# Kernel optimization log

Hardware: AMD Instinct MI355X
Metric: run time of the kernel (lower is better)

## Reference

```python
import jax, jax.numpy as jnp
import numpy as np

N_NODES = 100000
D = 128
ATT = 128
P_EDGE_TYPES = 3
N_EDGES = 1600000
BATCH = 65536


def gcn_conv(x, W, b, src, dst, n):
    # PyG GCNConv: add self loops, symmetric D^{-1/2} (A+I) D^{-1/2} x W + b
    h = x @ W                                   # [N, D]
    ones = jnp.ones(src.shape[0], x.dtype)
    deg = jax.ops.segment_sum(ones, dst, num_segments=n) + 1.0  # +1 self loop
    dinv = jax.lax.rsqrt(deg)
    norm = dinv[src] * dinv[dst]                # [E]
    out = jax.ops.segment_sum(h[src] * norm[:, None], dst, num_segments=n)
    out = out + h * (dinv * dinv)[:, None]      # self-loop message, norm = dinv_i^2
    return out + b


def semantic_attention(z, P, W, b, q):
    # z: [P*N, D] -> per-edge-type scalar attention, softmax over P, weighted sum
    att = jnp.tanh(z @ W + b) @ q               # [P*N]
    att = att.reshape(P, -1).mean(axis=1)       # [P]
    att = jax.nn.softmax(att)
    zp = z.reshape(P, -1, z.shape[-1])          # [P, N, D]
    return jnp.einsum('p,pnd->nd', att, zp)     # [N, D]


def gnn_branch(x0, edge_index, W1, b1, W2, b2, n):
    outs = []
    for t in range(edge_index.shape[0]):        # fixed small set of edge types
        src, dst = edge_index[t, 0], edge_index[t, 1]
        h = jax.nn.relu(gcn_conv(x0, W1, b1, src, dst, n))
        h = jax.nn.relu(gcn_conv(h, W2, b2, src, dst, n))
        outs.append(h)
    return jnp.concatenate(outs, axis=0)        # [P*N, D]


def setup_inputs() -> dict:
    key = jax.random.key(0)
    ks = jax.random.split(key, 16)
    x = jax.random.normal(ks[0], (N_NODES, D), jnp.float32)
    edge_index = jax.random.randint(ks[1], (P_EDGE_TYPES, 2, N_EDGES), 0, N_NODES, jnp.int64)
    perm = jax.random.permutation(ks[2], N_NODES).astype(jnp.int64)
    summary_vetor = jax.random.normal(ks[3], (D,), jnp.float32)
    s = 1.0 / np.sqrt(D)
    params = dict(
        W_lin=jax.random.normal(ks[4], (D, D), jnp.float32) * s,
        b_lin=jnp.zeros((D,), jnp.float32),
        W1=jax.random.normal(ks[5], (D, D), jnp.float32) * s,
        b1=jnp.zeros((D,), jnp.float32),
        W2=jax.random.normal(ks[6], (D, D), jnp.float32) * s,
        b2=jnp.zeros((D,), jnp.float32),
        W_sem=jax.random.normal(ks[7], (D, ATT), jnp.float32) * s,
        b_sem=jnp.zeros((ATT,), jnp.float32),
        q_sem=jax.random.normal(ks[8], (ATT,), jnp.float32) * (1.0 / np.sqrt(ATT)),
        W_disc=jax.random.normal(ks[9], (D, D), jnp.float32) * s,
        b_disc=jnp.zeros((), jnp.float32),
    )
    return dict(x=x, edge_index=edge_index, perm=perm,
                summary_vetor=summary_vetor, Batch_size=BATCH, **params)


def reference(x, edge_index, perm, summary_vetor, Batch_size,
              W_lin, b_lin, W1, b1, W2, b2, W_sem, b_sem, q_sem, W_disc, b_disc):
    n = x.shape[0]
    x_pos = jax.nn.relu(x @ W_lin + b_lin)
    x_neg = jax.nn.relu(x[perm] @ W_lin + b_lin)

    z_pos = gnn_branch(x_pos, edge_index, W1, b1, W2, b2, n)
    z_neg = gnn_branch(x_neg, edge_index, W1, b1, W2, b2, n)

    P = edge_index.shape[0]
    att_pos = semantic_attention(z_pos, P, W_sem, b_sem, q_sem)[:Batch_size]
    att_neg = semantic_attention(z_neg, P, W_sem, b_sem, q_sem)[:Batch_size]

    summary_in = att_pos.mean(axis=0)           # AvgReadout
    summary = 0.5 * (summary_vetor + summary_in)

    # Discriminator: bilinear score against broadcast summary
    c = W_disc @ summary                        # [D]
    sc_pos = att_pos @ c + b_disc               # [B]
    sc_neg = att_neg @ c + b_disc               # [B]
    ret = jnp.concatenate([sc_pos, sc_neg], axis=0)  # [2B]
    return ret, summary
```

## Files before the change

### kernel.cpp

```cpp
#include <hip/hip_runtime.h>

#define D_ 128
#define BATCH_ 65536
#define BSH 10
#define TILE_ 16384

typedef _Float16 f16;
typedef _Float16 h2v __attribute__((ext_vector_type(2)));
typedef _Float16 h4v __attribute__((ext_vector_type(4)));
typedef _Float16 f16x8 __attribute__((ext_vector_type(8)));
typedef float f32x4 __attribute__((ext_vector_type(4)));

__global__ void k_zero32(uint32_t* p, long long n) {
    long long i = (long long)blockIdx.x * blockDim.x + threadIdx.x;
    long long st = (long long)gridDim.x * blockDim.x;
    for (; i < n; i += st) p[i] = 0u;
}

__global__ void k_sentinel(float* p, long long n) {
    long long i = (long long)blockIdx.x * blockDim.x + threadIdx.x;
    long long st = (long long)gridDim.x * blockDim.x;
    for (; i < n; i += st) p[i] = -12345.0f;
}

__global__ void k_wt(const float* __restrict__ W, f16* __restrict__ Wt) {
    int t = blockIdx.x * 256 + threadIdx.x;
    int k = t >> 7, c = t & 127;
    Wt[c * 128 + k] = (f16)W[k * 128 + c];
}

__global__ void k_gath(const uint32_t* __restrict__ src, const int* __restrict__ perm,
                       uint32_t* __restrict__ dst, int N) {
    int i = blockIdx.x * 256 + threadIdx.x;
    if (i >= N * 64) return;
    int row = i >> 6, col = i & 63;
    dst[i] = src[((size_t)perm[row] << 6) + col];
}

__global__ void k_hist(const int* __restrict__ ei, int* __restrict__ bcnt,
                       int E, int nbt, int nbuk) {
    __shared__ int hist[512];
    for (int i = threadIdx.x; i < 512; i += 256) hist[i] = 0;
    __syncthreads();
    long long tot = 3LL * E;
    long long i = (long long)blockIdx.x * 256 + threadIdx.x;
    long long st = (long long)gridDim.x * 256;
    for (; i < tot; i += st) {
        int t = (i >= E) + (i >= 2LL * E);
        long long w = i - (long long)t * E;
        int dst = ei[(long long)t * 2 * E + E + w];
        atomicAdd(&hist[t * nbt + (dst >> BSH)], 1);
    }
    __syncthreads();
    for (int i2 = threadIdx.x; i2 < nbuk; i2 += 256)
        if (hist[i2]) atomicAdd(&bcnt[i2], hist[i2]);
}

__global__ void k_bscan(const int* __restrict__ bcnt, int* __restrict__ bbase,
                        int* __restrict__ bcur, int nbuk) {
    __shared__ int s[512];
    int t = threadIdx.x;
    int v = (t < nbuk) ? bcnt[t] : 0;
    s[t] = v;
    __syncthreads();
    for (int off = 1; off < 512; off <<= 1) {
        int a = (t >= off) ? s[t - off] : 0;
        __syncthreads();
        s[t] += a;
        __syncthreads();
    }
    if (t < nbuk) {
        int e = s[t] - v;
        bbase[t] = e;
        bcur[t] = e;
        if (t == nbuk - 1) bbase[nbuk] = s[t];
    }
}

__global__ __launch_bounds__(256) void k_scatter(const int* __restrict__ ei,
                                                 int* __restrict__ bcur,
                                                 uint32_t* __restrict__ pairs,
                                                 int E, int nbt, int nbuk) {
    __shared__ int hist[512];
    __shared__ int base[512];
    long long tot = 3LL * E;
    long long w0 = (long long)blockIdx.x * TILE_;
    long long w1 = w0 + TILE_ < tot ? w0 + TILE_ : tot;
    for (int i = threadIdx.x; i < 512; i += 256) hist[i] = 0;
    __syncthreads();
    for (long long e = w0 + threadIdx.x; e < w1; e += 256) {
        int t = (e >= E) + (e >= 2LL * E);
        long long w = e - (long long)t * E;
        int dst = ei[(long long)t * 2 * E + E + w];
        atomicAdd(&hist[t * nbt + (dst >> BSH)], 1);
    }
    __syncthreads();
    for (int i = threadIdx.x; i < nbuk; i += 256) {
        int c = hist[i];
        base[i] = c ? atomicAdd(&bcur[i], c) : 0;
        hist[i] = 0;
    }
    __syncthreads();
    for (long long e = w0 + threadIdx.x; e < w1; e += 256) {
        int t = (e >= E) + (e >= 2LL * E);
        long long w = e - (long long)t * E;
        int src = ei[(long long)t * 2 * E + w];
        int dst = ei[(long long)t * 2 * E + E + w];
        int b = t * nbt + (dst >> BSH);
        int off = atomicAdd(&hist[b], 1);
        pairs[base[b] + off] = (uint32_t)src | ((uint32_t)(dst & ((1 << BSH) - 1)) << 22);
    }
}

__global__ __launch_bounds__(256) void k_bucket(const uint32_t* __restrict__ pairs,
                                                const int* __restrict__ bbase,
                                                int* __restrict__ rowstart,
                                                float* __restrict__ dinv,
                                                int* __restrict__ csr,
                                                int N, int nbt, int nbuk, int L) {
    __shared__ int cnt[1024];
    __shared__ int pref[1024];
    __shared__ int sums[256];
    int b = blockIdx.x;
    int t = b / nbt, bb = b - t * nbt;
    int dst0 = bb << BSH;
    int ndst = (N - dst0 < 1024) ? (N - dst0) : 1024;
    int e0 = bbase[b], e1 = bbase[b + 1];
    int tid = threadIdx.x;
    for (int i = tid; i < 1024; i += 256) cnt[i] = 0;
    __syncthreads();
    for (int e = e0 + tid; e < e1; e += 256) atomicAdd(&cnt[pairs[e] >> 22], 1);
    __syncthreads();
    int i0 = tid * 4;
    int c0 = cnt[i0], c1 = cnt[i0 + 1], c2 = cnt[i0 + 2], c3 = cnt[i0 + 3];
    int s4 = c0 + c1 + c2 + c3;
    sums[tid] = s4;
    __syncthreads();
    for (int off = 1; off < 256; off <<= 1) {
        int v = (tid >= off) ? sums[tid - off] : 0;
        __syncthreads();
        sums[tid] += v;
        __syncthreads();
    }
    int run = sums[tid] - s4;
    pref[i0] = run; run += c0;
    pref[i0 + 1] = run; run += c1;
    pref[i0 + 2] = run; run += c2;
    pref[i0 + 3] = run;
    __syncthreads();
    for (int d = tid; d < ndst; d += 256) {
        int r = t * N + dst0 + d;
        rowstart[r] = e0 + pref[d];
        dinv[r] = rsqrtf((float)cnt[d] + 1.0f);
    }
    if (b == nbuk - 1 && tid == 0) rowstart[L] = e1;
    __syncthreads();
    for (int e = e0 + tid; e < e1; e += 256) {
        uint32_t u = pairs[e];
        int d = u >> 22;
        int pos = e0 + atomicAdd(&pref[d], 1);
        csr[pos] = (int)(u & ((1u << 22) - 1));
    }
}

__global__ void k_wedge(const int* __restrict__ csr, const float* __restrict__ dinv,
                        f16* __restrict__ w16, int N, int E) {
    long long tot = 3LL * E;
    long long i = (long long)blockIdx.x * 256 + threadIdx.x;
    long long st = (long long)gridDim.x * 256;
    for (; i < tot; i += st) {
        int t = (i >= E) + (i >= 2LL * E);
        w16[i] = (f16)dinv[t * N + csr[i]];
    }
}

__global__ __launch_bounds__(256) void k_mgemm(const void* __restrict__ in, int in_f32,
                                               const f16* __restrict__ Wt,
                                               const float* __restrict__ bias,
                                               f16* __restrict__ outh, int n, int relu) {
    int l = threadIdx.x & 63, wid = threadIdx.x >> 6;
    int row0 = blockIdx.x * 64 + wid * 16;
    int r = l & 15, kg = l >> 4;
    int arow = row0 + r;
    f32x4 acc[8] = {};
#pragma unroll
    for (int kk = 0; kk < 4; kk++) {
        int off = kk * 32 + kg * 8;
        f16x8 a = {};
        if (arow < n) {
            if (in_f32) {
                const float* inf = (const float*)in + (size_t)arow * D_ + off;
                float4 v0 = *(const float4*)inf;
                float4 v1 = *(const float4*)(inf + 4);
                a[0] = (f16)v0.x; a[1] = (f16)v0.y; a[2] = (f16)v0.z; a[3] = (f16)v0.w;
                a[4] = (f16)v1.x; a[5] = (f16)v1.y; a[6] = (f16)v1.z; a[7] = (f16)v1.w;
            } else {
                a = *(const f16x8*)((const f16*)in + (size_t)arow * D_ + off);
            }
        }
#pragma unroll
        for (int ct = 0; ct < 8; ct++) {
            int c = ct * 16 + r;
            f16x8 b = *(const f16x8*)(Wt + (size_t)c * D_ + off);
            acc[ct] = __builtin_amdgcn_mfma_f32_16x16x32_f16(a, b, acc[ct], 0, 0, 0);
        }
    }
#pragma unroll
    for (int ct = 0; ct < 8; ct++) {
        int c = ct * 16 + r;
        float bs = bias ? bias[c] : 0.0f;
#pragma unroll
        for (int j = 0; j < 4; j++) {
            int rr = row0 + kg * 4 + j;
            if (rr >= n) continue;
            float o = acc[ct][j] + bs;
            if (relu) o = fmaxf(o, 0.0f);
            outh[(size_t)rr * D_ + c] = (f16)o;
        }
    }
}

__global__ __launch_bounds__(256) void k_matt(const f16* __restrict__ z,
                                              const f16* __restrict__ Wst,
                                              const float* __restrict__ bsem,
                                              const float* __restrict__ q,
                                              float* __restrict__ att_part, int n, int ttype) {
    int l = threadIdx.x & 63, wid = threadIdx.x >> 6;
    int row0 = blockIdx.x * 64 + wid * 16;
    int r = l & 15, kg = l >> 4;
    int arow = row0 + r;
    f32x4 acc[8] = {};
#pragma unroll
    for (int kk = 0; kk < 4; kk++) {
        int off = kk * 32 + kg * 8;
        f16x8 a = {};
        if (arow < n) a = *(const f16x8*)(z + (size_t)arow * D_ + off);
#pragma unroll
        for (int ct = 0; ct < 8; ct++) {
            int c = ct * 16 + r;
            f16x8 b = *(const f16x8*)(Wst + (size_t)c * D_ + off);
            acc[ct] = __builtin_amdgcn_mfma_f32_16x16x32_f16(a, b, acc[ct], 0, 0, 0);
        }
    }
    float s = 0.0f;
#pragma unroll
    for (int ct = 0; ct < 8; ct++) {
        int c = ct * 16 + r;
        float qc = q[c], bc = bsem[c];
#pragma unroll
        for (int j = 0; j < 4; j++) {
            int rr = row0 + kg * 4 + j;
            if (rr < n) s += qc * tanhf(acc[ct][j] + bc);
        }
    }
#pragma unroll
    for (int m = 1; m < 64; m <<= 1) s += __shfl_xor(s, m, 64);
    __shared__ float ws[4];
    if (l == 0) ws[wid] = s;
    __syncthreads();
    if (threadIdx.x == 0)
        atomicAdd(&att_part[((blockIdx.x & 63) << 2) + ttype], ws[0] + ws[1] + ws[2] + ws[3]);
}

__global__ __launch_bounds__(256) void k_spmm(const f16* __restrict__ gsrc,
                                              const int* __restrict__ csr,
                                              const f16* __restrict__ w16,
                                              const int* __restrict__ rowstart,
                                              const float* __restrict__ dinv,
                                              const float* __restrict__ bias,
                                              f16* __restrict__ outh,
                                              int N, int rows, int src_typed) {
    int tid = (int)threadIdx.x;
    int lp = tid & 15;
    int gw = blockIdx.x * 16 + (tid >> 4);
    if (gw >= rows) return;
    int t = (gw >= N) + (gw >= 2 * N);
    int tbase = t * N;
    int sbase = src_typed ? tbase : 0;
    int self = src_typed ? gw : gw - tbase;
    int s0 = rowstart[gw], s1 = rowstart[gw + 1];
    float di = dinv[gw];
    size_t co = (size_t)(lp << 3);
    const f16* gp = gsrc + co;
    float a[8];
    {
        f16x8 sv = *(const f16x8*)(gp + (size_t)self * D_);
#pragma unroll
        for (int u = 0; u < 8; u++) a[u] = (float)sv[u] * di;
    }
    int j = s0;
    for (; j + 2 <= s1; j += 2) {
        int sA = csr[j], sB = csr[j + 1];
        float wA = (float)w16[j], wB = (float)w16[j + 1];
        f16x8 vA = *(const f16x8*)(gp + (size_t)(sbase + sA) * D_);
        f16x8 vB = *(const f16x8*)(gp + (size_t)(sbase + sB) * D_);
#pragma unroll
        for (int u = 0; u < 8; u++) a[u] = fmaf((float)vA[u], wA, a[u]);
#pragma unroll
        for (int u = 0; u < 8; u++) a[u] = fmaf((float)vB[u], wB, a[u]);
    }
    if (j < s1) {
        int s = csr[j];
        float w = (float)w16[j];
        f16x8 v = *(const f16x8*)(gp + (size_t)(sbase + s) * D_);
#pragma unroll
        for (int u = 0; u < 8; u++) a[u] = fmaf((float)v[u], w, a[u]);
    }
    float4 b0 = *(const float4*)(bias + co);
    float4 b1 = *(const float4*)(bias + co + 4);
    f16x8 o;
    o[0] = (f16)fmaxf(fmaf(a[0], di, b0.x), 0.f);
    o[1] = (f16)fmaxf(fmaf(a[1], di, b0.y), 0.f);
    o[2] = (f16)fmaxf(fmaf(a[2], di, b0.z), 0.f);
    o[3] = (f16)fmaxf(fmaf(a[3], di, b0.w), 0.f);
    o[4] = (f16)fmaxf(fmaf(a[4], di, b1.x), 0.f);
    o[5] = (f16)fmaxf(fmaf(a[5], di, b1.y), 0.f);
    o[6] = (f16)fmaxf(fmaf(a[6], di, b1.z), 0.f);
    o[7] = (f16)fmaxf(fmaf(a[7], di, b1.w), 0.f);
    *(f16x8*)(outh + (size_t)gw * D_ + co) = o;
}

__global__ void k_attw(const float* __restrict__ att_part, float* __restrict__ att_w, float invN) {
    __shared__ float sb[3];
    int t = threadIdx.x;
    if (t < 3) {
        float s = 0.f;
        for (int i = 0; i < 64; i++) s += att_part[(i << 2) + t];
        sb[t] = s * invN;
    }
    __syncthreads();
    if (t == 0) {
        float m = fmaxf(sb[0], fmaxf(sb[1], sb[2]));
        float x0 = expf(sb[0] - m), x1 = expf(sb[1] - m), x2 = expf(sb[2] - m);
        float inv = 1.f / (x0 + x1 + x2);
        att_w[0] = x0 * inv; att_w[1] = x1 * inv; att_w[2] = x2 * inv;
    }
}

__global__ __launch_bounds__(256) void k_colsum(const f16* __restrict__ Z, size_t tstride,
                                                const float* __restrict__ att_w,
                                                float* __restrict__ colsum) {
    int c2 = threadIdx.x & 63;
    int rg = threadIdx.x >> 6;
    int nbase = blockIdx.x << 7;
    float w0 = att_w[0], w1 = att_w[1], w2 = att_w[2];
    float csx = 0.f, csy = 0.f;
    for (int i = rg; i < 128; i += 4) {
        size_t off = (size_t)(nbase + i) * D_ + (c2 << 1);
        h2v z0 = *(const h2v*)(Z + off);
        h2v z1 = *(const h2v*)(Z + tstride + off);
        h2v z2 = *(const h2v*)(Z + 2 * tstride + off);
        csx += w0 * (float)z0.x + w1 * (float)z1.x + w2 * (float)z2.x;
        csy += w0 * (float)z0.y + w1 * (float)z1.y + w2 * (float)z2.y;
    }
    __shared__ float red[4][128];
    red[rg][c2 << 1] = csx;
    red[rg][(c2 << 1) + 1] = csy;
    __syncthreads();
    if (rg == 0) {
        float sx = red[0][c2 << 1] + red[1][c2 << 1] + red[2][c2 << 1] + red[3][c2 << 1];
        float sy = red[0][(c2 << 1) + 1] + red[1][(c2 << 1) + 1] + red[2][(c2 << 1) + 1] + red[3][(c2 << 1) + 1];
        atomicAdd(&colsum[c2 << 1], sx);
        atomicAdd(&colsum[(c2 << 1) + 1], sy);
    }
}

__global__ void k_summary_c(const float* __restrict__ colsum, const float* __restrict__ sv,
                            const float* __restrict__ Wd, float* __restrict__ cvec,
                            float* __restrict__ out_summary) {
    __shared__ float sl[128];
    int t = threadIdx.x;
    float s = 0.5f * (sv[t] + colsum[t] * (1.0f / (float)BATCH_));
    sl[t] = s;
    out_summary[t] = s;
    __syncthreads();
    float a = 0.f;
    for (int j = 0; j < 128; j++) a = fmaf(Wd[t * D_ + j], sl[j], a);
    cvec[t] = a;
}

__global__ __launch_bounds__(256) void k_cscore(const f16* __restrict__ Z, size_t tstride,
                                                const float* __restrict__ att_w,
                                                const float* __restrict__ c,
                                                const float* __restrict__ bd,
                                                float* __restrict__ out, int B) {
    int gw = (int)((blockIdx.x * (long long)blockDim.x + threadIdx.x) >> 6);
    int lane = threadIdx.x & 63;
    if (gw >= B) return;
    size_t off = (size_t)gw * D_ + (lane << 1);
    float w0 = att_w[0], w1 = att_w[1], w2 = att_w[2];
    h2v z0 = *(const h2v*)(Z + off);
    h2v z1 = *(const h2v*)(Z + tstride + off);
    h2v z2 = *(const h2v*)(Z + 2 * tstride + off);
    float vx = w0 * (float)z0.x + w1 * (float)z1.x + w2 * (float)z2.x;
    float vy = w0 * (float)z0.y + w1 * (float)z1.y + w2 * (float)z2.y;
    float2 cc = *(const float2*)(c + (lane << 1));
    float a = vx * cc.x + vy * cc.y;
#pragma unroll
    for (int m = 1; m < 64; m <<= 1) a += __shfl_xor(a, m, 64);
    if (lane == 0) out[gw] = a + bd[0];
}

extern "C" void kernel_launch(void* const* d_in, const int* in_sizes, int n_in,
                              void* d_out, int out_size, void* d_ws, size_t ws_size,
                              hipStream_t stream) {
    const float* x      = (const float*)d_in[0];
    const int*   ei     = (const int*)d_in[1];
    const int*   perm   = (const int*)d_in[2];
    const float* sv     = (const float*)d_in[3];
    const float* W_lin  = (const float*)d_in[5];
    const float* b_lin  = (const float*)d_in[6];
    const float* W1     = (const float*)d_in[7];
    const float* b1     = (const float*)d_in[8];
    const float* W2     = (const float*)d_in[9];
    const float* b2     = (const float*)d_in[10];
    const float* W_sem  = (const float*)d_in[11];
    const float* b_sem  = (const float*)d_in[12];
    const float* q_sem  = (const float*)d_in[13];
    const float* W_disc = (const float*)d_in[14];
    const float* b_disc = (const float*)d_in[15];
    float* out = (float*)d_out;

    int N = in_sizes[0] / D_;
    int E = in_sizes[1] / 6;
    int L = 3 * N;
    size_t ND = (size_t)N * D_;
    int B = BATCH_;
    int nbt = (N + (1 << BSH) - 1) >> BSH;
    int nbuk = 3 * nbt;

    char* ws = (char*)d_ws;
    size_t o = 0;
    auto alloc = [&](size_t bytes) -> char* {
        char* p = ws + o;
        o = (o + bytes + 255) & ~(size_t)255;
        return p;
    };
    float* dinv     = (float*)alloc((size_t)L * 4);
    int*   rowstart = (int*)alloc(((size_t)L + 1) * 4);
    int*   csr      = (int*)alloc(((size_t)3 * E + 16) * 4);
    int*   bcnt     = (int*)alloc(512 * 4);
    int*   bbase    = (int*)alloc(513 * 4);
    int*   bcur     = (int*)alloc(512 * 4);
    float* att_part = (float*)alloc(256 * 4);
    float* att_w    = (float*)alloc(16 * 4);
    float* colsum   = (float*)alloc(128 * 4);
    float* cvec     = (float*)alloc(128 * 4);
    f16*   Wlt      = (f16*)alloc(128 * 128 * 2);
    f16*   W1t      = (f16*)alloc(128 * 128 * 2);
    f16*   W2t      = (f16*)alloc(128 * 128 * 2);
    f16*   Wst      = (f16*)alloc(128 * 128 * 2);
    f16*   Ah       = (f16*)alloc(ND * 2);
    f16*   G1h      = (f16*)alloc(ND * 2);
    f16*   G1p      = (f16*)alloc(ND * 2);
    f16*   H1all    = (f16*)alloc(3 * ND * 2);
    f16*   Zall     = (f16*)alloc(3 * ND * 2);
    size_t o_full = o;

    uint32_t* pairs = (uint32_t*)Zall;
    f16*      w16  = (f16*)Ah;

    if (o_full > ws_size || N >= (1 << 22) || nbuk > 512 ||
        (size_t)3 * E * 4 > 3 * ND * 2 || (size_t)3 * E * 2 > ND * 2) {
        k_sentinel<<<256, 256, 0, stream>>>(out, out_size);
        return;
    }

    k_wt<<<64, 256, 0, stream>>>(W_lin, Wlt);
    k_wt<<<64, 256, 0, stream>>>(W1, W1t);
    k_wt<<<64, 256, 0, stream>>>(W2, W2t);
    k_wt<<<64, 256, 0, stream>>>(W_sem, Wst);

    long long tot = 3LL * E;
    k_zero32<<<2, 256, 0, stream>>>((uint32_t*)bcnt, 512);
    k_hist<<<2048, 256, 0, stream>>>(ei, bcnt, E, nbt, nbuk);
    k_bscan<<<1, 512, 0, stream>>>(bcnt, bbase, bcur, nbuk);
    int scat_grid = (int)((tot + TILE_ - 1) / TILE_);
    k_scatter<<<scat_grid, 256, 0, stream>>>(ei, bcur, pairs, E, nbt, nbuk);
    k_bucket<<<nbuk, 256, 0, stream>>>(pairs, bbase, rowstart, dinv, csr, N, nbt, nbuk, L);

    int mgN_grid  = (N + 63) / 64;
    int mgL_grid  = (L + 63) / 64;
    int spmm_grid = (L + 15) / 16;
    int scoreB_grid = (B + 3) / 4;

    k_mgemm<<<mgN_grid, 256, 0, stream>>>(x, 1, Wlt, b_lin, Ah, N, 1);
    k_mgemm<<<mgN_grid, 256, 0, stream>>>(Ah, 0, W1t, nullptr, G1h, N, 0);
    k_gath<<<(N * 64 + 255) / 256, 256, 0, stream>>>((const uint32_t*)G1h, perm,
                                                     (uint32_t*)G1p, N);
    k_wedge<<<2048, 256, 0, stream>>>(csr, dinv, w16, N, E);

    for (int br = 0; br < 2; br++) {
        const f16* src1 = br ? G1p : G1h;
        float* aw = att_w + br * 8;
        k_zero32<<<1, 256, 0, stream>>>((uint32_t*)att_part, 256);
        k_spmm<<<spmm_grid, 256, 0, stream>>>(src1, csr, w16, rowstart, dinv, b1,
                                              H1all, N, L, 0);
        k_mgemm<<<mgL_grid, 256, 0, stream>>>(H1all, 0, W2t, nullptr, H1all, L, 0);
        k_spmm<<<spmm_grid, 256, 0, stream>>>(H1all, csr, w16, rowstart, dinv, b2,
                                              Zall, N, L, 1);
        for (int t3 = 0; t3 < 3; t3++)
            k_matt<<<mgN_grid, 256, 0, stream>>>(Zall + (size_t)t3 * ND, Wst, b_sem, q_sem,
                                                 att_part, N, t3);
        k_attw<<<1, 64, 0, stream>>>(att_part, aw, 1.0f / (float)N);
        if (br == 0) {
            k_zero32<<<1, 256, 0, stream>>>((uint32_t*)colsum, 128);
            k_colsum<<<512, 256, 0, stream>>>(Zall, ND, aw, colsum);
            k_summary_c<<<1, 128, 0, stream>>>(colsum, sv, W_disc, cvec, out + 2 * (size_t)B);
            k_cscore<<<scoreB_grid, 256, 0, stream>>>(Zall, ND, aw, cvec, b_disc, out, B);
        } else {
            k_cscore<<<scoreB_grid, 256, 0, stream>>>(Zall, ND, aw, cvec, b_disc, out + B, B);
        }
    }
}
```

Measured before the change: 1.495 ms.

## Split SpMM aggregation into two passes by source-node half for locality

The CSR build now sorts each destination row's edges by whether the source index falls in the lower or upper half of the nodes, and records a mid-row offset. Each SpMM is launched twice: the first pass covers lower-half sources and writes an unbiased f16 partial sum. The second pass reloads that partial, adds the upper-half sources, then applies the normalisation, bias and ReLU. The aim is to halve the gathered feature working set per pass so more of it stays in cache. The cost is an extra round trip of the output through memory, an extra launch per layer, and f16 rounding of the intermediate partial sum.

```diff
diff --git a/kernel.cpp b/kernel.cpp
--- a/kernel.cpp
+++ b/kernel.cpp
@@ -7,7 +7,6 @@
 
 typedef _Float16 f16;
 typedef _Float16 h2v __attribute__((ext_vector_type(2)));
-typedef _Float16 h4v __attribute__((ext_vector_type(4)));
 typedef _Float16 f16x8 __attribute__((ext_vector_type(8)));
 typedef float f32x4 __attribute__((ext_vector_type(4)));
 
@@ -115,11 +114,12 @@
 __global__ __launch_bounds__(256) void k_bucket(const uint32_t* __restrict__ pairs,
                                                 const int* __restrict__ bbase,
                                                 int* __restrict__ rowstart,
+                                                int* __restrict__ rowmid,
                                                 float* __restrict__ dinv,
                                                 int* __restrict__ csr,
-                                                int N, int nbt, int nbuk, int L) {
-    __shared__ int cnt[1024];
-    __shared__ int pref[1024];
+                                                int N, int Nhalf, int nbt, int nbuk, int L) {
+    __shared__ int cnt[2048];
+    __shared__ int pref[2048];
     __shared__ int sums[256];
     int b = blockIdx.x;
     int t = b / nbt, bb = b - t * nbt;
@@ -127,14 +127,20 @@
     int ndst = (N - dst0 < 1024) ? (N - dst0) : 1024;
     int e0 = bbase[b], e1 = bbase[b + 1];
     int tid = threadIdx.x;
-    for (int i = tid; i < 1024; i += 256) cnt[i] = 0;
-    __syncthreads();
-    for (int e = e0 + tid; e < e1; e += 256) atomicAdd(&cnt[pairs[e] >> 22], 1);
-    __syncthreads();
-    int i0 = tid * 4;
-    int c0 = cnt[i0], c1 = cnt[i0 + 1], c2 = cnt[i0 + 2], c3 = cnt[i0 + 3];
-    int s4 = c0 + c1 + c2 + c3;
-    sums[tid] = s4;
+    for (int i = tid; i < 2048; i += 256) cnt[i] = 0;
+    __syncthreads();
+    for (int e = e0 + tid; e < e1; e += 256) {
+        uint32_t u = pairs[e];
+        int d = u >> 22;
+        int src = (int)(u & ((1u << 22) - 1));
+        atomicAdd(&cnt[(d << 1) | (src >= Nhalf)], 1);
+    }
+    __syncthreads();
+    int i0 = tid * 8;
+    int c[8], s8 = 0;
+#pragma unroll
+    for (int u = 0; u < 8; u++) { c[u] = cnt[i0 + u]; s8 += c[u]; }
+    sums[tid] = s8;
     __syncthreads();
     for (int off = 1; off < 256; off <<= 1) {
         int v = (tid >= off) ? sums[tid - off] : 0;
@@ -142,24 +148,25 @@
         sums[tid] += v;
         __syncthreads();
     }
-    int run = sums[tid] - s4;
-    pref[i0] = run; run += c0;
-    pref[i0 + 1] = run; run += c1;
-    pref[i0 + 2] = run; run += c2;
-    pref[i0 + 3] = run;
+    int run = sums[tid] - s8;
+#pragma unroll
+    for (int u = 0; u < 8; u++) { pref[i0 + u] = run; run += c[u]; }
     __syncthreads();
     for (int d = tid; d < ndst; d += 256) {
         int r = t * N + dst0 + d;
-        rowstart[r] = e0 + pref[d];
-        dinv[r] = rsqrtf((float)cnt[d] + 1.0f);
+        rowstart[r] = e0 + pref[2 * d];
+        rowmid[r]   = e0 + pref[2 * d + 1];
+        dinv[r] = rsqrtf((float)(cnt[2 * d] + cnt[2 * d + 1]) + 1.0f);
     }
     if (b == nbuk - 1 && tid == 0) rowstart[L] = e1;
     __syncthreads();
     for (int e = e0 + tid; e < e1; e += 256) {
         uint32_t u = pairs[e];
         int d = u >> 22;
-        int pos = e0 + atomicAdd(&pref[d], 1);
-        csr[pos] = (int)(u & ((1u << 22) - 1));
+        int src = (int)(u & ((1u << 22) - 1));
+        int key = (d << 1) | (src >= Nhalf);
+        int pos = e0 + atomicAdd(&pref[key], 1);
+        csr[pos] = src;
     }
 }
 
@@ -265,11 +272,12 @@
 __global__ __launch_bounds__(256) void k_spmm(const f16* __restrict__ gsrc,
                                               const int* __restrict__ csr,
                                               const f16* __restrict__ w16,
-                                              const int* __restrict__ rowstart,
+                                              const int* __restrict__ jb,
+                                              const int* __restrict__ je,
                                               const float* __restrict__ dinv,
                                               const float* __restrict__ bias,
                                               f16* __restrict__ outh,
-                                              int N, int rows, int src_typed) {
+                                              int N, int rows, int src_typed, int final_) {
     int tid = (int)threadIdx.x;
     int lp = tid & 15;
     int gw = blockIdx.x * 16 + (tid >> 4);
@@ -277,13 +285,18 @@
     int t = (gw >= N) + (gw >= 2 * N);
     int tbase = t * N;
     int sbase = src_typed ? tbase : 0;
-    int self = src_typed ? gw : gw - tbase;
-    int s0 = rowstart[gw], s1 = rowstart[gw + 1];
+    int s0 = jb[gw], s1 = je[gw];
     float di = dinv[gw];
     size_t co = (size_t)(lp << 3);
     const f16* gp = gsrc + co;
+    f16* op = outh + (size_t)gw * D_ + co;
     float a[8];
-    {
+    if (final_) {
+        f16x8 pv = *(const f16x8*)op;
+#pragma unroll
+        for (int u = 0; u < 8; u++) a[u] = (float)pv[u];
+    } else {
+        int self = src_typed ? gw : gw - tbase;
         f16x8 sv = *(const f16x8*)(gp + (size_t)self * D_);
 #pragma unroll
         for (int u = 0; u < 8; u++) a[u] = (float)sv[u] * di;
@@ -306,18 +319,23 @@
 #pragma unroll
         for (int u = 0; u < 8; u++) a[u] = fmaf((float)v[u], w, a[u]);
     }
-    float4 b0 = *(const float4*)(bias + co);
-    float4 b1 = *(const float4*)(bias + co + 4);
     f16x8 o;
-    o[0] = (f16)fmaxf(fmaf(a[0], di, b0.x), 0.f);
-    o[1] = (f16)fmaxf(fmaf(a[1], di, b0.y), 0.f);
-    o[2] = (f16)fmaxf(fmaf(a[2], di, b0.z), 0.f);
-    o[3] = (f16)fmaxf(fmaf(a[3], di, b0.w), 0.f);
-    o[4] = (f16)fmaxf(fmaf(a[4], di, b1.x), 0.f);
-    o[5] = (f16)fmaxf(fmaf(a[5], di, b1.y), 0.f);
-    o[6] = (f16)fmaxf(fmaf(a[6], di, b1.z), 0.f);
-    o[7] = (f16)fmaxf(fmaf(a[7], di, b1.w), 0.f);
-    *(f16x8*)(outh + (size_t)gw * D_ + co) = o;
+    if (final_) {
+        float4 b0 = *(const float4*)(bias + co);
+        float4 b1 = *(const float4*)(bias + co + 4);
+        o[0] = (f16)fmaxf(fmaf(a[0], di, b0.x), 0.f);
+        o[1] = (f16)fmaxf(fmaf(a[1], di, b0.y), 0.f);
+        o[2] = (f16)fmaxf(fmaf(a[2], di, b0.z), 0.f);
+        o[3] = (f16)fmaxf(fmaf(a[3], di, b0.w), 0.f);
+        o[4] = (f16)fmaxf(fmaf(a[4], di, b1.x), 0.f);
+        o[5] = (f16)fmaxf(fmaf(a[5], di, b1.y), 0.f);
+        o[6] = (f16)fmaxf(fmaf(a[6], di, b1.z), 0.f);
+        o[7] = (f16)fmaxf(fmaf(a[7], di, b1.w), 0.f);
+    } else {
+#pragma unroll
+        for (int u = 0; u < 8; u++) o[u] = (f16)a[u];
+    }
+    *(f16x8*)op = o;
 }
 
 __global__ void k_attw(const float* __restrict__ att_part, float* __restrict__ att_w, float invN) {
@@ -428,6 +446,7 @@
     int B = BATCH_;
     int nbt = (N + (1 << BSH) - 1) >> BSH;
     int nbuk = 3 * nbt;
+    int Nhalf = N / 2;
 
     char* ws = (char*)d_ws;
     size_t o = 0;
@@ -438,6 +457,7 @@
     };
     float* dinv     = (float*)alloc((size_t)L * 4);
     int*   rowstart = (int*)alloc(((size_t)L + 1) * 4);
+    int*   rowmid   = (int*)alloc(((size_t)L + 1) * 4);
     int*   csr      = (int*)alloc(((size_t)3 * E + 16) * 4);
     int*   bcnt     = (int*)alloc(512 * 4);
     int*   bbase    = (int*)alloc(513 * 4);
@@ -477,7 +497,8 @@
     k_bscan<<<1, 512, 0, stream>>>(bcnt, bbase, bcur, nbuk);
     int scat_grid = (int)((tot + TILE_ - 1) / TILE_);
     k_scatter<<<scat_grid, 256, 0, stream>>>(ei, bcur, pairs, E, nbt, nbuk);
-    k_bucket<<<nbuk, 256, 0, stream>>>(pairs, bbase, rowstart, dinv, csr, N, nbt, nbuk, L);
+    k_bucket<<<nbuk, 256, 0, stream>>>(pairs, bbase, rowstart, rowmid, dinv, csr,
+                                       N, Nhalf, nbt, nbuk, L);
 
     int mgN_grid  = (N + 63) / 64;
     int mgL_grid  = (L + 63) / 64;
@@ -494,11 +515,15 @@
         const f16* src1 = br ? G1p : G1h;
         float* aw = att_w + br * 8;
         k_zero32<<<1, 256, 0, stream>>>((uint32_t*)att_part, 256);
-        k_spmm<<<spmm_grid, 256, 0, stream>>>(src1, csr, w16, rowstart, dinv, b1,
-                                              H1all, N, L, 0);
+        k_spmm<<<spmm_grid, 256, 0, stream>>>(src1, csr, w16, rowstart, rowmid, dinv, b1,
+                                              H1all, N, L, 0, 0);
+        k_spmm<<<spmm_grid, 256, 0, stream>>>(src1, csr, w16, rowmid, rowstart + 1, dinv, b1,
+                                              H1all, N, L, 0, 1);
         k_mgemm<<<mgL_grid, 256, 0, stream>>>(H1all, 0, W2t, nullptr, H1all, L, 0);
-        k_spmm<<<spmm_grid, 256, 0, stream>>>(H1all, csr, w16, rowstart, dinv, b2,
-                                              Zall, N, L, 1);
+        k_spmm<<<spmm_grid, 256, 0, stream>>>(H1all, csr, w16, rowstart, rowmid, dinv, b2,
+                                              Zall, N, L, 1, 0);
+        k_spmm<<<spmm_grid, 256, 0, stream>>>(H1all, csr, w16, rowmid, rowstart + 1, dinv, b2,
+                                              Zall, N, L, 1, 1);
         for (int t3 = 0; t3 < 3; t3++)
             k_matt<<<mgN_grid, 256, 0, stream>>>(Zall + (size_t)t3 * ND, Wst, b_sem, q_sem,
                                                  att_part, N, t3);
```

Result: slower. 1.574 ms (+5.2%).

## Double rows per wave in MFMA GEMMs and merge per-type attention launches

Applied to the files above, without the earlier changes.

Each wave in the dense GEMM and semantic-attention kernels now computes 32 rows instead of 16, reusing each loaded weight fragment for two MFMAs and halving the grid. The three per-edge-type attention launches are merged into one launch over all 3N rows, with each 16-row group picking its edge type from its row index and doing its own atomic add. This cuts redundant weight loads and launch overhead, at the cost of more accumulator registers and more atomics. A guard now requires N to be a multiple of 16 so that no 16-row group spans two edge types.

```diff
diff --git a/kernel.cpp b/kernel.cpp
--- a/kernel.cpp
+++ b/kernel.cpp
@@ -7,7 +7,6 @@
 
 typedef _Float16 f16;
 typedef _Float16 h2v __attribute__((ext_vector_type(2)));
-typedef _Float16 h4v __attribute__((ext_vector_type(4)));
 typedef _Float16 f16x8 __attribute__((ext_vector_type(8)));
 typedef float f32x4 __attribute__((ext_vector_type(4)));
 
@@ -179,43 +178,51 @@
                                                const float* __restrict__ bias,
                                                f16* __restrict__ outh, int n, int relu) {
     int l = threadIdx.x & 63, wid = threadIdx.x >> 6;
-    int row0 = blockIdx.x * 64 + wid * 16;
+    int row0 = blockIdx.x * 128 + wid * 32;
     int r = l & 15, kg = l >> 4;
-    int arow = row0 + r;
-    f32x4 acc[8] = {};
+    f32x4 acc[2][8] = {};
 #pragma unroll
     for (int kk = 0; kk < 4; kk++) {
         int off = kk * 32 + kg * 8;
-        f16x8 a = {};
-        if (arow < n) {
-            if (in_f32) {
-                const float* inf = (const float*)in + (size_t)arow * D_ + off;
-                float4 v0 = *(const float4*)inf;
-                float4 v1 = *(const float4*)(inf + 4);
-                a[0] = (f16)v0.x; a[1] = (f16)v0.y; a[2] = (f16)v0.z; a[3] = (f16)v0.w;
-                a[4] = (f16)v1.x; a[5] = (f16)v1.y; a[6] = (f16)v1.z; a[7] = (f16)v1.w;
-            } else {
-                a = *(const f16x8*)((const f16*)in + (size_t)arow * D_ + off);
+        f16x8 a[2];
+#pragma unroll
+        for (int h = 0; h < 2; h++) {
+            int arow = row0 + h * 16 + r;
+            f16x8 av = {};
+            if (arow < n) {
+                if (in_f32) {
+                    const float* inf = (const float*)in + (size_t)arow * D_ + off;
+                    float4 v0 = *(const float4*)inf;
+                    float4 v1 = *(const float4*)(inf + 4);
+                    av[0] = (f16)v0.x; av[1] = (f16)v0.y; av[2] = (f16)v0.z; av[3] = (f16)v0.w;
+                    av[4] = (f16)v1.x; av[5] = (f16)v1.y; av[6] = (f16)v1.z; av[7] = (f16)v1.w;
+                } else {
+                    av = *(const f16x8*)((const f16*)in + (size_t)arow * D_ + off);
+                }
             }
-        }
+            a[h] = av;
+        }
+#pragma unroll
+        for (int ct = 0; ct < 8; ct++) {
+            f16x8 b = *(const f16x8*)(Wt + (size_t)(ct * 16 + r) * D_ + off);
+            acc[0][ct] = __builtin_amdgcn_mfma_f32_16x16x32_f16(a[0], b, acc[0][ct], 0, 0, 0);
+            acc[1][ct] = __builtin_amdgcn_mfma_f32_16x16x32_f16(a[1], b, acc[1][ct], 0, 0, 0);
+        }
+    }
+#pragma unroll
+    for (int h = 0; h < 2; h++) {
 #pragma unroll
         for (int ct = 0; ct < 8; ct++) {
             int c = ct * 16 + r;
-            f16x8 b = *(const f16x8*)(Wt + (size_t)c * D_ + off);
-            acc[ct] = __builtin_amdgcn_mfma_f32_16x16x32_f16(a, b, acc[ct], 0, 0, 0);
-        }
-    }
-#pragma unroll
-    for (int ct = 0; ct < 8; ct++) {
-        int c = ct * 16 + r;
-        float bs = bias ? bias[c] : 0.0f;
-#pragma unroll
-        for (int j = 0; j < 4; j++) {
-            int rr = row0 + kg * 4 + j;
-            if (rr >= n) continue;
-            float o = acc[ct][j] + bs;
-            if (relu) o = fmaxf(o, 0.0f);
-            outh[(size_t)rr * D_ + c] = (f16)o;
+            float bs = bias ? bias[c] : 0.0f;
+#pragma unroll
+            for (int j = 0; j < 4; j++) {
+                int rr = row0 + h * 16 + kg * 4 + j;
+                if (rr >= n) continue;
+                float o = acc[h][ct][j] + bs;
+                if (relu) o = fmaxf(o, 0.0f);
+                outh[(size_t)rr * D_ + c] = (f16)o;
+            }
         }
     }
 }
@@ -224,42 +231,51 @@
                                               const f16* __restrict__ Wst,
                                               const float* __restrict__ bsem,
                                               const float* __restrict__ q,
-                                              float* __restrict__ att_part, int n, int ttype) {
+                                              float* __restrict__ att_part, int N, int rows) {
     int l = threadIdx.x & 63, wid = threadIdx.x >> 6;
-    int row0 = blockIdx.x * 64 + wid * 16;
+    int row0 = blockIdx.x * 128 + wid * 32;
     int r = l & 15, kg = l >> 4;
-    int arow = row0 + r;
-    f32x4 acc[8] = {};
+    f32x4 acc[2][8] = {};
 #pragma unroll
     for (int kk = 0; kk < 4; kk++) {
         int off = kk * 32 + kg * 8;
-        f16x8 a = {};
-        if (arow < n) a = *(const f16x8*)(z + (size_t)arow * D_ + off);
+        f16x8 a[2];
+#pragma unroll
+        for (int h = 0; h < 2; h++) {
+            int arow = row0 + h * 16 + r;
+            f16x8 av = {};
+            if (arow < rows) av = *(const f16x8*)(z + (size_t)arow * D_ + off);
+            a[h] = av;
+        }
+#pragma unroll
+        for (int ct = 0; ct < 8; ct++) {
+            f16x8 b = *(const f16x8*)(Wst + (size_t)(ct * 16 + r) * D_ + off);
+            acc[0][ct] = __builtin_amdgcn_mfma_f32_16x16x32_f16(a[0], b, acc[0][ct], 0, 0, 0);
+            acc[1][ct] = __builtin_amdgcn_mfma_f32_16x16x32_f16(a[1], b, acc[1][ct], 0, 0, 0);
+        }
+    }
+#pragma unroll
+    for (int h = 0; h < 2; h++) {
+        int rowh = row0 + h * 16;
+        if (rowh >= rows) continue;
+        float s = 0.0f;
 #pragma unroll
         for (int ct = 0; ct < 8; ct++) {
             int c = ct * 16 + r;
-            f16x8 b = *(const f16x8*)(Wst + (size_t)c * D_ + off);
-            acc[ct] = __builtin_amdgcn_mfma_f32_16x16x32_f16(a, b, acc[ct], 0, 0, 0);
-        }
-    }
-    float s = 0.0f;
-#pragma unroll
-    for (int ct = 0; ct < 8; ct++) {
-        int c = ct * 16 + r;
-        float qc = q[c], bc = bsem[c];
-#pragma unroll
-        for (int j = 0; j < 4; j++) {
-            int rr = row0 + kg * 4 + j;
-            if (rr < n) s += qc * tanhf(acc[ct][j] + bc);
-        }
-    }
-#pragma unroll
-    for (int m = 1; m < 64; m <<= 1) s += __shfl_xor(s, m, 64);
-    __shared__ float ws[4];
-    if (l == 0) ws[wid] = s;
-    __syncthreads();
-    if (threadIdx.x == 0)
-        atomicAdd(&att_part[((blockIdx.x & 63) << 2) + ttype], ws[0] + ws[1] + ws[2] + ws[3]);
+            float qc = q[c], bc = bsem[c];
+#pragma unroll
+            for (int j = 0; j < 4; j++) {
+                int rr = rowh + kg * 4 + j;
+                if (rr < rows) s += qc * tanhf(acc[h][ct][j] + bc);
+            }
+        }
+#pragma unroll
+        for (int m = 1; m < 64; m <<= 1) s += __shfl_xor(s, m, 64);
+        if (l == 0) {
+            int t = (rowh >= N) + (rowh >= 2 * N);
+            atomicAdd(&att_part[((blockIdx.x & 63) << 2) + t], s);
+        }
+    }
 }
 
 __global__ __launch_bounds__(256) void k_spmm(const f16* __restrict__ gsrc,
@@ -460,7 +476,7 @@
     uint32_t* pairs = (uint32_t*)Zall;
     f16*      w16  = (f16*)Ah;
 
-    if (o_full > ws_size || N >= (1 << 22) || nbuk > 512 ||
+    if (o_full > ws_size || N >= (1 << 22) || (N & 15) || nbuk > 512 ||
         (size_t)3 * E * 4 > 3 * ND * 2 || (size_t)3 * E * 2 > ND * 2) {
         k_sentinel<<<256, 256, 0, stream>>>(out, out_size);
         return;
@@ -479,8 +495,8 @@
     k_scatter<<<scat_grid, 256, 0, stream>>>(ei, bcur, pairs, E, nbt, nbuk);
     k_bucket<<<nbuk, 256, 0, stream>>>(pairs, bbase, rowstart, dinv, csr, N, nbt, nbuk, L);
 
-    int mgN_grid  = (N + 63) / 64;
-    int mgL_grid  = (L + 63) / 64;
+    int mgN_grid  = (N + 127) / 128;
+    int mgL_grid  = (L + 127) / 128;
     int spmm_grid = (L + 15) / 16;
     int scoreB_grid = (B + 3) / 4;
 
@@ -499,9 +515,7 @@
         k_mgemm<<<mgL_grid, 256, 0, stream>>>(H1all, 0, W2t, nullptr, H1all, L, 0);
         k_spmm<<<spmm_grid, 256, 0, stream>>>(H1all, csr, w16, rowstart, dinv, b2,
                                               Zall, N, L, 1);
-        for (int t3 = 0; t3 < 3; t3++)
-            k_matt<<<mgN_grid, 256, 0, stream>>>(Zall + (size_t)t3 * ND, Wst, b_sem, q_sem,
-                                                 att_part, N, t3);
+        k_matt<<<mgL_grid, 256, 0, stream>>>(Zall, Wst, b_sem, q_sem, att_part, N, L);
         k_attw<<<1, 64, 0, stream>>>(att_part, aw, 1.0f / (float)N);
         if (br == 0) {
             k_zero32<<<1, 256, 0, stream>>>((uint32_t*)colsum, 128);
```

Result: faster. 1.411 ms (-5.7%).
